# Kernel optimization log

Hardware: AMD Instinct MI355X
Metric: run time of the kernel (lower is better)

Reference implementation:

```python
import jax, jax.numpy as jnp
import numpy as np

NEG_SLOPE = 0.2  # PyG GATConv default negative_slope


def _add_self_loops(edge_index, num_nodes):
    # PyG GATConv add_self_loops=True default
    loop = jnp.arange(num_nodes, dtype=edge_index.dtype)
    src = jnp.concatenate([edge_index[0], loop])
    dst = jnp.concatenate([edge_index[1], loop])
    return src, dst


def _gat_layer(x, src, dst, W, att_src, att_dst, bias, heads, out_ch):
    """One PyG-style GATConv layer (concat=True).
    x: [N, F_in]; W: [F_in, heads*out_ch]; att_*: [heads, out_ch]; bias: [heads*out_ch].
    """
    N = x.shape[0]
    h = (x @ W).reshape(N, heads, out_ch)               # [N, H, C]
    a_src = jnp.einsum('nhc,hc->nh', h, att_src)        # [N, H]
    a_dst = jnp.einsum('nhc,hc->nh', h, att_dst)        # [N, H]
    logits = jax.nn.leaky_relu(a_src[src] + a_dst[dst], NEG_SLOPE)  # [E, H]
    # segment softmax over destination neighborhoods
    m = jax.ops.segment_max(logits, dst, num_segments=N)            # [N, H]
    e = jnp.exp(logits - m[dst])                                     # [E, H]
    s = jax.ops.segment_sum(e, dst, num_segments=N)                  # [N, H]
    alpha = e / s[dst]                                               # [E, H]
    # scatter-aggregate weighted source features
    out = jax.ops.segment_sum(alpha[:, :, None] * h[src], dst, num_segments=N)  # [N, H, C]
    return out.reshape(N, heads * out_ch) + bias


def setup_inputs() -> dict:
    key = jax.random.key(0)
    ks = jax.random.split(key, 10)
    N, E = 50000, 800000
    F_in, HID, H, NC = 128, 64, 4, 10
    x = jax.random.normal(ks[0], (N, F_in), dtype=jnp.float32)
    edge_index = jax.random.randint(ks[1], (2, E), 0, N, dtype=jnp.int64)
    sc1 = 1.0 / np.sqrt(F_in)
    sc2 = 1.0 / np.sqrt(HID * H)
    return {
        'x': x,
        'edge_index': edge_index,
        'W1': jax.random.normal(ks[2], (F_in, H * HID), dtype=jnp.float32) * sc1,
        'att_src1': jax.random.normal(ks[3], (H, HID), dtype=jnp.float32) * sc1,
        'att_dst1': jax.random.normal(ks[4], (H, HID), dtype=jnp.float32) * sc1,
        'b1': jnp.zeros((H * HID,), dtype=jnp.float32),
        'W2': jax.random.normal(ks[5], (H * HID, NC), dtype=jnp.float32) * sc2,
        'att_src2': jax.random.normal(ks[6], (1, NC), dtype=jnp.float32) * sc2,
        'att_dst2': jax.random.normal(ks[7], (1, NC), dtype=jnp.float32) * sc2,
        'b2': jnp.zeros((NC,), dtype=jnp.float32),
    }


def reference(x, edge_index, W1, att_src1, att_dst1, b1, W2, att_src2, att_dst2, b2):
    N = x.shape[0]
    src, dst = _add_self_loops(edge_index, N)
    h = _gat_layer(x, src, dst, W1, att_src1, att_dst1, b1, heads=4, out_ch=64)
    h = jax.nn.elu(h)
    out = _gat_layer(h, src, dst, W2, att_src2, att_dst2, b2, heads=1, out_ch=10)
    return out
```

## Files before the change

### kernel.cpp

```cpp
#include <hip/hip_runtime.h>
#include <hip/hip_fp16.h>
#include <math.h>

#define NEG_SLOPE 0.2f
#define LOG2E 1.44269504088896f

#if __has_builtin(__builtin_amdgcn_exp2f)
#define EXP2(x) __builtin_amdgcn_exp2f(x)
#else
#define EXP2(x) exp2f(x)
#endif

typedef _Float16 half8 __attribute__((ext_vector_type(8)));
typedef float floatx4 __attribute__((ext_vector_type(4)));

__global__ __launch_bounds__(256) void prep1(const float* __restrict__ W1,
                                             half8* __restrict__ Bpack,
                                             int* __restrict__ deg, int N) {
  if (blockIdx.x < 16) {
    int tid = blockIdx.x * 256 + threadIdx.x;
    int l = tid & 63;
    int ksnt = tid >> 6;
    int ks = ksnt & 3;
    int nt = ksnt >> 2;
    int col = nt * 16 + (l & 15);
    int krow = ks * 32 + (l >> 4) * 8;
    half8 v;
#pragma unroll
    for (int j = 0; j < 8; j++) v[j] = (_Float16)W1[(krow + j) * 256 + col];
    Bpack[tid] = v;
  } else {
    int i = (blockIdx.x - 16) * 256 + threadIdx.x;
    if (i < N) deg[i] = 0;
  }
}

__global__ __launch_bounds__(256) void phase2(
    const float* __restrict__ x, const half8* __restrict__ Bpack,
    const float* __restrict__ att_s, const float* __restrict__ att_d,
    unsigned char* __restrict__ h1q, float* __restrict__ a1sx,
    float* __restrict__ a1d,
    const int* __restrict__ dst, int* __restrict__ deg, int* __restrict__ rank,
    int N, int E, int gemmBlocks, int histBlocks) {
  if ((int)blockIdx.x >= gemmBlocks) {
    int b = blockIdx.x - gemmBlocks;
    for (int e = b * 256 + threadIdx.x; e < E; e += histBlocks * 256)
      rank[e] = atomicAdd(deg + dst[e], 1);
    return;
  }
  const int wave = threadIdx.x >> 6, lane = threadIdx.x & 63;
  const int quad = lane >> 4, li = lane & 15;
  const int n0 = (blockIdx.x * 4 + wave) * 16;
  if (n0 >= N) return;
  floatx4 acc[16];
#pragma unroll
  for (int t = 0; t < 16; t++) acc[t] = (floatx4){0.f, 0.f, 0.f, 0.f};
  const float* xrow = x + (size_t)(n0 + li) * 128;
#pragma unroll
  for (int ks = 0; ks < 4; ks++) {
    float4 xa = *(const float4*)(xrow + ks * 32 + quad * 8);
    float4 xb = *(const float4*)(xrow + ks * 32 + quad * 8 + 4);
    half8 a;
    a[0] = (_Float16)xa.x; a[1] = (_Float16)xa.y;
    a[2] = (_Float16)xa.z; a[3] = (_Float16)xa.w;
    a[4] = (_Float16)xb.x; a[5] = (_Float16)xb.y;
    a[6] = (_Float16)xb.z; a[7] = (_Float16)xb.w;
#pragma unroll
    for (int nt = 0; nt < 16; nt++) {
      half8 b = Bpack[(nt * 4 + ks) * 64 + lane];
      acc[nt] = __builtin_amdgcn_mfma_f32_16x16x32_f16(a, b, acc[nt], 0, 0, 0);
    }
  }
#pragma unroll
  for (int r = 0; r < 4; r++) {
    float m = 0.f;
#pragma unroll
    for (int nt = 0; nt < 16; nt++) m = fmaxf(m, fabsf(acc[nt][r]));
#pragma unroll
    for (int off = 8; off > 0; off >>= 1) m = fmaxf(m, __shfl_xor(m, off, 16));
    m = fmaxf(m, 1e-8f);
    float inv = 127.0f / m;
    int node = n0 + quad * 4 + r;
    if (li == 0) a1sx[(size_t)node * 8 + 4] = m * (1.0f / 127.0f);
#pragma unroll
    for (int nt = 0; nt < 16; nt++) {
      h1q[(size_t)node * 256 + nt * 16 + li] =
          (unsigned char)(int)(fmaf(acc[nt][r], inv, 128.5f));
    }
  }
  float as_f[16], ad_f[16];
#pragma unroll
  for (int nt = 0; nt < 16; nt++) {
    as_f[nt] = att_s[nt * 16 + li];
    ad_f[nt] = att_d[nt * 16 + li];
  }
#pragma unroll
  for (int r = 0; r < 4; r++) {
    int node = n0 + quad * 4 + r;
#pragma unroll
    for (int h = 0; h < 4; h++) {
      float vs = 0.f, vd = 0.f;
#pragma unroll
      for (int ntl = 0; ntl < 4; ntl++) {
        int nt = h * 4 + ntl;
        vs = fmaf(acc[nt][r], as_f[nt], vs);
        vd = fmaf(acc[nt][r], ad_f[nt], vd);
      }
#pragma unroll
      for (int off = 8; off > 0; off >>= 1) {
        vs += __shfl_down(vs, off, 16);
        vd += __shfl_down(vd, off, 16);
      }
      if (li == 0) {
        a1sx[(size_t)node * 8 + h] = vs * LOG2E;
        a1d[node * 4 + h] = vd * LOG2E;
      }
    }
  }
}

__global__ void scan_local(const int* __restrict__ deg, int* __restrict__ excl,
                           int* __restrict__ bsum, int N) {
  __shared__ int s[256];
  int i = blockIdx.x * 256 + threadIdx.x;
  int v = (i < N) ? deg[i] + 1 : 0;
  s[threadIdx.x] = v;
  __syncthreads();
  for (int off = 1; off < 256; off <<= 1) {
    int t = (threadIdx.x >= off) ? s[threadIdx.x - off] : 0;
    __syncthreads();
    s[threadIdx.x] += t;
    __syncthreads();
  }
  if (i < N) excl[i] = s[threadIdx.x] - v;
  if (threadIdx.x == 255) bsum[blockIdx.x] = s[255];
}

__global__ void scan_add2(const int* __restrict__ excl, const int* __restrict__ bsum,
                          int* __restrict__ rowptr, int* __restrict__ elist,
                          int N, int nb) {
  __shared__ int s[256];
  int v = (threadIdx.x < nb) ? bsum[threadIdx.x] : 0;
  s[threadIdx.x] = v;
  __syncthreads();
  for (int off = 1; off < 256; off <<= 1) {
    int t = (threadIdx.x >= off) ? s[threadIdx.x - off] : 0;
    __syncthreads();
    s[threadIdx.x] += t;
    __syncthreads();
  }
  __syncthreads();
  int base = (blockIdx.x > 0) ? s[blockIdx.x - 1] : 0;
  int i = blockIdx.x * 256 + threadIdx.x;
  if (i < N) {
    int r = excl[i] + base;
    rowptr[i] = r;
    elist[r] = i;
  }
  if (blockIdx.x == 0 && threadIdx.x == 0) rowptr[N] = s[nb - 1];
}

__global__ void scatter2(const int* __restrict__ src, const int* __restrict__ dst,
                         const int* __restrict__ rank, const int* __restrict__ rowptr,
                         int* __restrict__ elist, int E) {
  int e = blockIdx.x * 256 + threadIdx.x;
  if (e >= E) return;
  elist[rowptr[dst[e]] + 1 + rank[e]] = src[e];
}

__global__ __launch_bounds__(256) void agg1_fused(
    const int* __restrict__ rowptr, const int* __restrict__ elist,
    const unsigned char* __restrict__ h1q, const float* __restrict__ a1sx,
    const float* __restrict__ a1d,
    const float* __restrict__ b1, const float* __restrict__ W2,
    const float* __restrict__ as2, const float* __restrict__ ad2,
    __half* __restrict__ h2, int N) {
  __shared__ float w2s[64 * 41];
  __shared__ float cbuf[8][256];
  const int t = threadIdx.x;
  for (int i = t; i < 2560; i += 256) {
    int ch = i / 10, jj = i - ch * 10;
    w2s[(ch >> 2) * 41 + (ch & 3) * 10 + jj] = W2[i];
  }

  const int wave = t >> 6, lane = t & 63;
  const int half = lane >> 5, l32 = lane & 31;
  const int slot = wave * 2 + half;
  const int n = blockIdx.x * 8 + slot;
  const bool act = n < N;
  const int row = act ? rowptr[n] : 0;
  const int deg = act ? rowptr[n + 1] - row : 0;
  const int* el = elist + row;
  const int hidx = l32 >> 3;
  const float adh = act ? a1d[n * 4 + hidx] : 0.f;

  float den = 0.f, T = 0.f;
  float acc[8];
#pragma unroll
  for (int k = 0; k < 8; k++) acc[k] = 0.f;

  int j = 0;
  for (; j + 4 <= deg; j += 4) {
    int ss[4];
    float lv[4], sc[4];
    uint2 qv[4];
#pragma unroll
    for (int u = 0; u < 4; u++) ss[u] = el[j + u];
#pragma unroll
    for (int u = 0; u < 4; u++) {
      const float* mp = a1sx + (size_t)ss[u] * 8;
      lv[u] = mp[hidx];
      sc[u] = mp[4];
      qv[u] = *(const uint2*)(h1q + (size_t)ss[u] * 256 + l32 * 8);
    }
#pragma unroll
    for (int u = 0; u < 4; u++) {
      float l = lv[u] + adh;
      float e = EXP2(fmaxf(l, NEG_SLOPE * l));
      den += e;
      float se = e * sc[u];
      T += se;
      unsigned int a = qv[u].x, b = qv[u].y;
      acc[0] = fmaf((float)(a & 0xffu), se, acc[0]);
      acc[1] = fmaf((float)((a >> 8) & 0xffu), se, acc[1]);
      acc[2] = fmaf((float)((a >> 16) & 0xffu), se, acc[2]);
      acc[3] = fmaf((float)(a >> 24), se, acc[3]);
      acc[4] = fmaf((float)(b & 0xffu), se, acc[4]);
      acc[5] = fmaf((float)((b >> 8) & 0xffu), se, acc[5]);
      acc[6] = fmaf((float)((b >> 16) & 0xffu), se, acc[6]);
      acc[7] = fmaf((float)(b >> 24), se, acc[7]);
    }
  }
  for (; j < deg; j++) {
    int s0 = el[j];
    const float* mp = a1sx + (size_t)s0 * 8;
    float l0 = mp[hidx] + adh;
    float sc0 = mp[4];
    uint2 q0 = *(const uint2*)(h1q + (size_t)s0 * 256 + l32 * 8);
    float e0 = EXP2(fmaxf(l0, NEG_SLOPE * l0));
    den += e0;
    float se = e0 * sc0;
    T += se;
    unsigned int a = q0.x, b = q0.y;
    acc[0] = fmaf((float)(a & 0xffu), se, acc[0]);
    acc[1] = fmaf((float)((a >> 8) & 0xffu), se, acc[1]);
    acc[2] = fmaf((float)((a >> 16) & 0xffu), se, acc[2]);
    acc[3] = fmaf((float)(a >> 24), se, acc[3]);
    acc[4] = fmaf((float)(b & 0xffu), se, acc[4]);
    acc[5] = fmaf((float)((b >> 8) & 0xffu), se, acc[5]);
    acc[6] = fmaf((float)((b >> 16) & 0xffu), se, acc[6]);
    acc[7] = fmaf((float)(b >> 24), se, acc[7]);
  }

  if (act) {
    float inv = 1.0f / den;
    float corr = 128.0f * T;
    float4 v0 = make_float4((acc[0] - corr) * inv, (acc[1] - corr) * inv,
                            (acc[2] - corr) * inv, (acc[3] - corr) * inv);
    float4 v1 = make_float4((acc[4] - corr) * inv, (acc[5] - corr) * inv,
                            (acc[6] - corr) * inv, (acc[7] - corr) * inv);
    *(float4*)&cbuf[slot][l32 * 8] = v0;
    *(float4*)&cbuf[slot][l32 * 8 + 4] = v1;
  }
  __syncthreads();

  float4 bb = *(const float4*)(b1 + lane * 4);
  const float* w0 = w2s + lane * 41;
#pragma unroll
  for (int pp = 0; pp < 2; pp++) {
    int slot2 = wave * 2 + pp;
    int n2 = blockIdx.x * 8 + slot2;
    if (n2 >= N) continue;
    float4 cv = *(const float4*)&cbuf[slot2][lane * 4];
    float c0 = cv.x + bb.x;
    float c1 = cv.y + bb.y;
    float c2 = cv.z + bb.z;
    float c3 = cv.w + bb.w;
    c0 = c0 > 0.f ? c0 : expm1f(c0);
    c1 = c1 > 0.f ? c1 : expm1f(c1);
    c2 = c2 > 0.f ? c2 : expm1f(c2);
    c3 = c3 > 0.f ? c3 : expm1f(c3);
    float p[10];
#pragma unroll
    for (int jj = 0; jj < 10; jj++)
      p[jj] = fmaf(c0, w0[jj],
              fmaf(c1, w0[10 + jj], fmaf(c2, w0[20 + jj], c3 * w0[30 + jj])));
#pragma unroll
    for (int jj = 0; jj < 10; jj++) {
#pragma unroll
      for (int off = 32; off > 0; off >>= 1) p[jj] += __shfl_down(p[jj], off, 64);
    }
    if (lane == 0) {
      float ds = 0.f, dd = 0.f;
#pragma unroll
      for (int jj = 0; jj < 10; jj++) {
        h2[(size_t)n2 * 16 + jj] = __float2half(p[jj]);
        ds = fmaf(p[jj], as2[jj], ds);
        dd = fmaf(p[jj], ad2[jj], dd);
      }
      float* ft = (float*)(h2 + (size_t)n2 * 16);
      ft[5] = ds * LOG2E;
      ft[6] = dd * LOG2E;
    }
  }
}

__global__ __launch_bounds__(256) void agg2_csr(
    const int* __restrict__ rowptr, const int* __restrict__ elist,
    const __half* __restrict__ h2, const float* __restrict__ b2,
    float* __restrict__ out, int N) {
  int wave = threadIdx.x >> 6, lane = threadIdx.x & 63;
  int n = blockIdx.x * 4 + wave;
  if (n >= N) return;
  int row = rowptr[n];
  int deg = rowptr[n + 1] - row;
  const int* el = elist + row;
  const float* hf = (const float*)h2;
  float ad = hf[(size_t)n * 8 + 6];
  int g = lane / 5;
  int c2 = lane - g * 5;
  float den = 0.f, ax = 0.f, ay = 0.f;
  if (g < 12) {
    int jj = g;
    for (; jj + 12 < deg; jj += 24) {
      int sA = el[jj], sB = el[jj + 12];
      float lA = hf[(size_t)sA * 8 + 5] + ad;
      float lB = hf[(size_t)sB * 8 + 5] + ad;
      __half2 hA = *(const __half2*)(h2 + (size_t)sA * 16 + c2 * 2);
      __half2 hB = *(const __half2*)(h2 + (size_t)sB * 16 + c2 * 2);
      float eA = EXP2(fmaxf(lA, NEG_SLOPE * lA));
      float eB = EXP2(fmaxf(lB, NEG_SLOPE * lB));
      den += eA + eB;
      float2 fA = __half22float2(hA);
      float2 fB = __half22float2(hB);
      ax = fmaf(eA, fA.x, fmaf(eB, fB.x, ax));
      ay = fmaf(eA, fA.y, fmaf(eB, fB.y, ay));
    }
    for (; jj < deg; jj += 12) {
      int s = el[jj];
      float l = hf[(size_t)s * 8 + 5] + ad;
      __half2 hv = *(const __half2*)(h2 + (size_t)s * 16 + c2 * 2);
      float ev = EXP2(fmaxf(l, NEG_SLOPE * l));
      den += ev;
      float2 f = __half22float2(hv);
      ax = fmaf(ev, f.x, ax);
      ay = fmaf(ev, f.y, ay);
    }
  }
  ax += __shfl_down(ax, 30, 64);
  ay += __shfl_down(ay, 30, 64);
  den += __shfl_down(den, 30, 64);
  ax += __shfl_down(ax, 10, 64) + __shfl_down(ax, 20, 64);
  ay += __shfl_down(ay, 10, 64) + __shfl_down(ay, 20, 64);
  den += __shfl_down(den, 10, 64) + __shfl_down(den, 20, 64);
  ax += __shfl_down(ax, 5, 64);
  ay += __shfl_down(ay, 5, 64);
  den += __shfl_down(den, 5, 64);
  if (lane < 5) {
    float inv = 1.0f / den;
    float2 bb = *(const float2*)(b2 + lane * 2);
    float2 o = make_float2(fmaf(ax, inv, bb.x), fmaf(ay, inv, bb.y));
    *(float2*)(out + (size_t)n * 10 + lane * 2) = o;
  }
}

extern "C" void kernel_launch(void* const* d_in, const int* in_sizes, int n_in,
                              void* d_out, int out_size, void* d_ws, size_t ws_size,
                              hipStream_t stream) {
  const float* x = (const float*)d_in[0];
  const int* ei = (const int*)d_in[1];
  const float* W1 = (const float*)d_in[2];
  const float* as1 = (const float*)d_in[3];
  const float* ad1 = (const float*)d_in[4];
  const float* b1 = (const float*)d_in[5];
  const float* W2 = (const float*)d_in[6];
  const float* as2 = (const float*)d_in[7];
  const float* ad2 = (const float*)d_in[8];
  const float* b2 = (const float*)d_in[9];
  float* out = (float*)d_out;

  const int N = in_sizes[0] / 128;
  const int E = in_sizes[1] / 2;
  const int* srcp = ei;
  const int* dstp = ei + E;

  char* ws = (char*)d_ws;
  size_t off = 0;
  auto alloc = [&](size_t nbytes) {
    char* p = ws + off;
    off += (nbytes + 255) & ~(size_t)255;
    return p;
  };
  unsigned char* h1q = (unsigned char*)alloc((size_t)N * 256);
  float* a1sx = (float*)alloc((size_t)N * 8 * 4);
  half8* Bpack = (half8*)alloc((size_t)4096 * 16);
  float* a1d = (float*)alloc((size_t)N * 4 * 4);
  __half* h2 = (__half*)alloc((size_t)N * 16 * 2);
  int* deg = (int*)alloc((size_t)N * 4);
  int* excl = (int*)alloc((size_t)N * 4);
  int* bsum = (int*)alloc(256 * 4);
  int* rowptr = (int*)alloc((size_t)(N + 1) * 4);
  int* rank = (int*)alloc((size_t)E * 4);
  int* elist = (int*)alloc((size_t)(E + (size_t)N) * 4);

  const int nb = (N + 255) / 256;
  const int gemmBlocks = (N / 16 + 3) / 4;
  const int histBlocks = 512;

  prep1<<<16 + nb, 256, 0, stream>>>(W1, Bpack, deg, N);
  phase2<<<gemmBlocks + histBlocks, 256, 0, stream>>>(
      x, Bpack, as1, ad1, h1q, a1sx, a1d, dstp, deg, rank, N, E,
      gemmBlocks, histBlocks);
  scan_local<<<nb, 256, 0, stream>>>(deg, excl, bsum, N);
  scan_add2<<<nb, 256, 0, stream>>>(excl, bsum, rowptr, elist, N, nb);
  scatter2<<<(E + 255) / 256, 256, 0, stream>>>(srcp, dstp, rank, rowptr, elist, E);
  agg1_fused<<<(N + 7) / 8, 256, 0, stream>>>(rowptr, elist, h1q, a1sx, a1d,
                                              b1, W2, as2, ad2, h2, N);
  agg2_csr<<<(N + 3) / 4, 256, 0, stream>>>(rowptr, elist, h2, b2, out, N);
}
```

Measured before the change: 249.8 us.

## Embed per-source attention scalars into a 32-byte edge list record

Each CSR edge entry grows from a bare source index to a 32-byte record. The record holds the source's four head attention logits, its quantization scale and a precomputed byte offset into h1q. These are written during the scatter. The aggregation kernels then read the record sequentially instead of doing a dependent random gather into a1sx, and agg2 reuses the offset (shifted) to address h2. The trade is 8x more edge-list memory traffic and a larger scatter write, in exchange for one fewer dependent random load per edge; a launch_bounds occupancy hint is also added.

Result: slower. 264.0 us (+5.7%).

```diff
diff --git a/kernel.cpp b/kernel.cpp
--- a/kernel.cpp
+++ b/kernel.cpp
@@ -137,7 +137,8 @@
 }
 
 __global__ void scan_add2(const int* __restrict__ excl, const int* __restrict__ bsum,
-                          int* __restrict__ rowptr, int* __restrict__ elist,
+                          const float* __restrict__ a1sx,
+                          int* __restrict__ rowptr, char* __restrict__ elist2,
                           int N, int nb) {
   __shared__ int s[256];
   int v = (threadIdx.x < nb) ? bsum[threadIdx.x] : 0;
@@ -155,23 +156,33 @@
   if (i < N) {
     int r = excl[i] + base;
     rowptr[i] = r;
-    elist[r] = i;
+    float4 m0 = *(const float4*)(a1sx + (size_t)i * 8);
+    float sc = a1sx[(size_t)i * 8 + 4];
+    float4* ep = (float4*)(elist2 + (size_t)r * 32);
+    ep[0] = m0;
+    ep[1] = make_float4(sc, __int_as_float(i * 256), 0.f, 0.f);
   }
   if (blockIdx.x == 0 && threadIdx.x == 0) rowptr[N] = s[nb - 1];
 }
 
 __global__ void scatter2(const int* __restrict__ src, const int* __restrict__ dst,
                          const int* __restrict__ rank, const int* __restrict__ rowptr,
-                         int* __restrict__ elist, int E) {
+                         const float* __restrict__ a1sx, char* __restrict__ elist2,
+                         int E) {
   int e = blockIdx.x * 256 + threadIdx.x;
   if (e >= E) return;
-  elist[rowptr[dst[e]] + 1 + rank[e]] = src[e];
-}
-
-__global__ __launch_bounds__(256) void agg1_fused(
-    const int* __restrict__ rowptr, const int* __restrict__ elist,
-    const unsigned char* __restrict__ h1q, const float* __restrict__ a1sx,
-    const float* __restrict__ a1d,
+  int s = src[e];
+  int r = rowptr[dst[e]] + 1 + rank[e];
+  float4 m0 = *(const float4*)(a1sx + (size_t)s * 8);
+  float sc = a1sx[(size_t)s * 8 + 4];
+  float4* ep = (float4*)(elist2 + (size_t)r * 32);
+  ep[0] = m0;
+  ep[1] = make_float4(sc, __int_as_float(s * 256), 0.f, 0.f);
+}
+
+__global__ __launch_bounds__(256, 4) void agg1_fused(
+    const int* __restrict__ rowptr, const char* __restrict__ elist2,
+    const unsigned char* __restrict__ h1q, const float* __restrict__ a1d,
     const float* __restrict__ b1, const float* __restrict__ W2,
     const float* __restrict__ as2, const float* __restrict__ ad2,
     __half* __restrict__ h2, int N) {
@@ -190,10 +201,12 @@
   const bool act = n < N;
   const int row = act ? rowptr[n] : 0;
   const int deg = act ? rowptr[n + 1] - row : 0;
-  const int* el = elist + row;
   const int hidx = l32 >> 3;
   const float adh = act ? a1d[n * 4 + hidx] : 0.f;
 
+  const float4* eb = (const float4*)(elist2) + (size_t)row * 2;
+  const unsigned char* h1ql = h1q + l32 * 8;
+
   float den = 0.f, T = 0.f;
   float acc[8];
 #pragma unroll
@@ -201,24 +214,24 @@
 
   int j = 0;
   for (; j + 4 <= deg; j += 4) {
-    int ss[4];
-    float lv[4], sc[4];
+    float4 ea[4], es[4];
     uint2 qv[4];
 #pragma unroll
-    for (int u = 0; u < 4; u++) ss[u] = el[j + u];
-#pragma unroll
     for (int u = 0; u < 4; u++) {
-      const float* mp = a1sx + (size_t)ss[u] * 8;
-      lv[u] = mp[hidx];
-      sc[u] = mp[4];
-      qv[u] = *(const uint2*)(h1q + (size_t)ss[u] * 256 + l32 * 8);
-    }
+      ea[u] = eb[(size_t)(j + u) * 2];
+      es[u] = eb[(size_t)(j + u) * 2 + 1];
+    }
+#pragma unroll
+    for (int u = 0; u < 4; u++)
+      qv[u] = *(const uint2*)(h1ql + (size_t)__float_as_uint(es[u].y));
 #pragma unroll
     for (int u = 0; u < 4; u++) {
-      float l = lv[u] + adh;
+      float lh = (hidx & 2) ? ((hidx & 1) ? ea[u].w : ea[u].z)
+                            : ((hidx & 1) ? ea[u].y : ea[u].x);
+      float l = lh + adh;
       float e = EXP2(fmaxf(l, NEG_SLOPE * l));
       den += e;
-      float se = e * sc[u];
+      float se = e * es[u].x;
       T += se;
       unsigned int a = qv[u].x, b = qv[u].y;
       acc[0] = fmaf((float)(a & 0xffu), se, acc[0]);
@@ -232,14 +245,15 @@
     }
   }
   for (; j < deg; j++) {
-    int s0 = el[j];
-    const float* mp = a1sx + (size_t)s0 * 8;
-    float l0 = mp[hidx] + adh;
-    float sc0 = mp[4];
-    uint2 q0 = *(const uint2*)(h1q + (size_t)s0 * 256 + l32 * 8);
+    float4 ea = eb[(size_t)j * 2];
+    float4 es = eb[(size_t)j * 2 + 1];
+    uint2 q0 = *(const uint2*)(h1ql + (size_t)__float_as_uint(es.y));
+    float lh = (hidx & 2) ? ((hidx & 1) ? ea.w : ea.z)
+                          : ((hidx & 1) ? ea.y : ea.x);
+    float l0 = lh + adh;
     float e0 = EXP2(fmaxf(l0, NEG_SLOPE * l0));
     den += e0;
-    float se = e0 * sc0;
+    float se = e0 * es.x;
     T += se;
     unsigned int a = q0.x, b = q0.y;
     acc[0] = fmaf((float)(a & 0xffu), se, acc[0]);
@@ -306,7 +320,7 @@
 }
 
 __global__ __launch_bounds__(256) void agg2_csr(
-    const int* __restrict__ rowptr, const int* __restrict__ elist,
+    const int* __restrict__ rowptr, const char* __restrict__ elist2,
     const __half* __restrict__ h2, const float* __restrict__ b2,
     float* __restrict__ out, int N) {
   int wave = threadIdx.x >> 6, lane = threadIdx.x & 63;
@@ -314,7 +328,8 @@
   if (n >= N) return;
   int row = rowptr[n];
   int deg = rowptr[n + 1] - row;
-  const int* el = elist + row;
+  const char* el2 = elist2 + (size_t)row * 32 + 20;
+  const char* h2b = (const char*)h2;
   const float* hf = (const float*)h2;
   float ad = hf[(size_t)n * 8 + 6];
   int g = lane / 5;
@@ -323,11 +338,14 @@
   if (g < 12) {
     int jj = g;
     for (; jj + 12 < deg; jj += 24) {
-      int sA = el[jj], sB = el[jj + 12];
-      float lA = hf[(size_t)sA * 8 + 5] + ad;
-      float lB = hf[(size_t)sB * 8 + 5] + ad;
-      __half2 hA = *(const __half2*)(h2 + (size_t)sA * 16 + c2 * 2);
-      __half2 hB = *(const __half2*)(h2 + (size_t)sB * 16 + c2 * 2);
+      unsigned oA = __float_as_uint(*(const float*)(el2 + (size_t)jj * 32));
+      unsigned oB = __float_as_uint(*(const float*)(el2 + (size_t)(jj + 12) * 32));
+      const float* rA = (const float*)(h2b + (oA >> 3));
+      const float* rB = (const float*)(h2b + (oB >> 3));
+      float lA = rA[5] + ad;
+      float lB = rB[5] + ad;
+      __half2 hA = *(const __half2*)((const char*)rA + c2 * 4);
+      __half2 hB = *(const __half2*)((const char*)rB + c2 * 4);
       float eA = EXP2(fmaxf(lA, NEG_SLOPE * lA));
       float eB = EXP2(fmaxf(lB, NEG_SLOPE * lB));
       den += eA + eB;
@@ -337,9 +355,10 @@
       ay = fmaf(eA, fA.y, fmaf(eB, fB.y, ay));
     }
     for (; jj < deg; jj += 12) {
-      int s = el[jj];
-      float l = hf[(size_t)s * 8 + 5] + ad;
-      __half2 hv = *(const __half2*)(h2 + (size_t)s * 16 + c2 * 2);
+      unsigned o = __float_as_uint(*(const float*)(el2 + (size_t)jj * 32));
+      const float* r = (const float*)(h2b + (o >> 3));
+      float l = r[5] + ad;
+      __half2 hv = *(const __half2*)((const char*)r + c2 * 4);
       float ev = EXP2(fmaxf(l, NEG_SLOPE * l));
       den += ev;
       float2 f = __half22float2(hv);
@@ -401,7 +420,7 @@
   int* bsum = (int*)alloc(256 * 4);
   int* rowptr = (int*)alloc((size_t)(N + 1) * 4);
   int* rank = (int*)alloc((size_t)E * 4);
-  int* elist = (int*)alloc((size_t)(E + (size_t)N) * 4);
+  char* elist2 = (char*)alloc((size_t)(E + (size_t)N) * 32);
 
   const int nb = (N + 255) / 256;
   const int gemmBlocks = (N / 16 + 3) / 4;
@@ -412,9 +431,10 @@
       x, Bpack, as1, ad1, h1q, a1sx, a1d, dstp, deg, rank, N, E,
       gemmBlocks, histBlocks);
   scan_local<<<nb, 256, 0, stream>>>(deg, excl, bsum, N);
-  scan_add2<<<nb, 256, 0, stream>>>(excl, bsum, rowptr, elist, N, nb);
-  scatter2<<<(E + 255) / 256, 256, 0, stream>>>(srcp, dstp, rank, rowptr, elist, E);
-  agg1_fused<<<(N + 7) / 8, 256, 0, stream>>>(rowptr, elist, h1q, a1sx, a1d,
+  scan_add2<<<nb, 256, 0, stream>>>(excl, bsum, a1sx, rowptr, elist2, N, nb);
+  scatter2<<<(E + 255) / 256, 256, 0, stream>>>(srcp, dstp, rank, rowptr, a1sx,
+                                                elist2, E);
+  agg1_fused<<<(N + 7) / 8, 256, 0, stream>>>(rowptr, elist2, h1q, a1d,
                                               b1, W2, as2, ad2, h2, N);
-  agg2_csr<<<(N + 3) / 4, 256, 0, stream>>>(rowptr, elist, h2, b2, out, N);
-}
+  agg2_csr<<<(N + 3) / 4, 256, 0, stream>>>(rowptr, elist2, h2, b2, out, N);
+}
```

## Partially sort CSR neighbor lists by source tile for gather locality

Applied to the files above, without the earlier changes.

Splits each destination's degree counter into eight buckets keyed by the high bits of the source index. The scatter then places edges grouped by source tile within each row, so neighbor lists are roughly ordered by source. This is meant to improve cache locality of the h1q and h2 feature gathers in the aggregation kernels. In exchange it uses a degree array eight times larger, with more zeroing, a wider read in the scan, and extra prefix work per edge in the scatter. Correctness depends on N fitting within eight tiles of 8192 sources.

Result: no change. 250.3 us (+0.2%).

```diff
diff --git a/kernel.cpp b/kernel.cpp
--- a/kernel.cpp
+++ b/kernel.cpp
@@ -13,6 +13,9 @@
 
 typedef _Float16 half8 __attribute__((ext_vector_type(8)));
 typedef float floatx4 __attribute__((ext_vector_type(4)));
+
+#define SRC_TILE_SHIFT 13
+#define NTILES 8
 
 __global__ __launch_bounds__(256) void prep1(const float* __restrict__ W1,
                                              half8* __restrict__ Bpack,
@@ -31,7 +34,7 @@
     Bpack[tid] = v;
   } else {
     int i = (blockIdx.x - 16) * 256 + threadIdx.x;
-    if (i < N) deg[i] = 0;
+    if (i < N * NTILES) deg[i] = 0;
   }
 }
 
@@ -40,12 +43,15 @@
     const float* __restrict__ att_s, const float* __restrict__ att_d,
     unsigned char* __restrict__ h1q, float* __restrict__ a1sx,
     float* __restrict__ a1d,
-    const int* __restrict__ dst, int* __restrict__ deg, int* __restrict__ rank,
+    const int* __restrict__ src, const int* __restrict__ dst,
+    int* __restrict__ deg, int* __restrict__ rank,
     int N, int E, int gemmBlocks, int histBlocks) {
   if ((int)blockIdx.x >= gemmBlocks) {
     int b = blockIdx.x - gemmBlocks;
-    for (int e = b * 256 + threadIdx.x; e < E; e += histBlocks * 256)
-      rank[e] = atomicAdd(deg + dst[e], 1);
+    for (int e = b * 256 + threadIdx.x; e < E; e += histBlocks * 256) {
+      int tile = src[e] >> SRC_TILE_SHIFT;
+      rank[e] = atomicAdd(deg + dst[e] * NTILES + tile, 1);
+    }
     return;
   }
   const int wave = threadIdx.x >> 6, lane = threadIdx.x & 63;
@@ -123,7 +129,12 @@
                            int* __restrict__ bsum, int N) {
   __shared__ int s[256];
   int i = blockIdx.x * 256 + threadIdx.x;
-  int v = (i < N) ? deg[i] + 1 : 0;
+  int v = 0;
+  if (i < N) {
+    const int4* dp = (const int4*)(deg + (size_t)i * NTILES);
+    int4 c0 = dp[0], c1 = dp[1];
+    v = c0.x + c0.y + c0.z + c0.w + c1.x + c1.y + c1.z + c1.w + 1;
+  }
   s[threadIdx.x] = v;
   __syncthreads();
   for (int off = 1; off < 256; off <<= 1) {
@@ -162,10 +173,19 @@
 
 __global__ void scatter2(const int* __restrict__ src, const int* __restrict__ dst,
                          const int* __restrict__ rank, const int* __restrict__ rowptr,
-                         int* __restrict__ elist, int E) {
+                         const int* __restrict__ deg, int* __restrict__ elist, int E) {
   int e = blockIdx.x * 256 + threadIdx.x;
   if (e >= E) return;
-  elist[rowptr[dst[e]] + 1 + rank[e]] = src[e];
+  int s = src[e];
+  int d = dst[e];
+  int tile = s >> SRC_TILE_SHIFT;
+  const int4* dp = (const int4*)(deg + (size_t)d * NTILES);
+  int4 c0 = dp[0], c1 = dp[1];
+  int cnt[8] = {c0.x, c0.y, c0.z, c0.w, c1.x, c1.y, c1.z, c1.w};
+  int pre = 0;
+#pragma unroll
+  for (int t = 0; t < 7; t++) pre += (t < tile) ? cnt[t] : 0;
+  elist[rowptr[d] + 1 + pre + rank[e]] = s;
 }
 
 __global__ __launch_bounds__(256) void agg1_fused(
@@ -396,7 +416,7 @@
   half8* Bpack = (half8*)alloc((size_t)4096 * 16);
   float* a1d = (float*)alloc((size_t)N * 4 * 4);
   __half* h2 = (__half*)alloc((size_t)N * 16 * 2);
-  int* deg = (int*)alloc((size_t)N * 4);
+  int* deg = (int*)alloc((size_t)N * NTILES * 4);
   int* excl = (int*)alloc((size_t)N * 4);
   int* bsum = (int*)alloc(256 * 4);
   int* rowptr = (int*)alloc((size_t)(N + 1) * 4);
@@ -404,16 +424,18 @@
   int* elist = (int*)alloc((size_t)(E + (size_t)N) * 4);
 
   const int nb = (N + 255) / 256;
+  const int nbz = (N * NTILES + 255) / 256;
   const int gemmBlocks = (N / 16 + 3) / 4;
   const int histBlocks = 512;
 
-  prep1<<<16 + nb, 256, 0, stream>>>(W1, Bpack, deg, N);
+  prep1<<<16 + nbz, 256, 0, stream>>>(W1, Bpack, deg, N);
   phase2<<<gemmBlocks + histBlocks, 256, 0, stream>>>(
-      x, Bpack, as1, ad1, h1q, a1sx, a1d, dstp, deg, rank, N, E,
+      x, Bpack, as1, ad1, h1q, a1sx, a1d, srcp, dstp, deg, rank, N, E,
       gemmBlocks, histBlocks);
   scan_local<<<nb, 256, 0, stream>>>(deg, excl, bsum, N);
   scan_add2<<<nb, 256, 0, stream>>>(excl, bsum, rowptr, elist, N, nb);
-  scatter2<<<(E + 255) / 256, 256, 0, stream>>>(srcp, dstp, rank, rowptr, elist, E);
+  scatter2<<<(E + 255) / 256, 256, 0, stream>>>(srcp, dstp, rank, rowptr, deg,
+                                                elist, E);
   agg1_fused<<<(N + 7) / 8, 256, 0, stream>>>(rowptr, elist, h1q, a1sx, a1d,
                                               b1, W2, as2, ad2, h2, N);
   agg2_csr<<<(N + 3) / 4, 256, 0, stream>>>(rowptr, elist, h2, b2, out, N);
```

## Split layer-1 aggregation per head with XCD-aware mapping and degree-sorted nodes

Applied to the files above, without the earlier changes.

Stores quantized h1 and per-head logit/scale in head-major planes so each head's gather touches a smaller contiguous array. Blocks are mapped so each XCD pair handles one head, which keeps that head's plane resident in the local L2. Nodes are counting-sorted by degree so wavefronts see balanced work. The layer-2 projection now goes through per-head partial sums and a new combine kernel, which adds launches, an N×40 float intermediate and atomics for binning.

After: 486.3 us. 1.95x slower.

```diff
diff --git a/kernel.cpp b/kernel.cpp
--- a/kernel.cpp
+++ b/kernel.cpp
@@ -16,7 +16,7 @@
 
 __global__ __launch_bounds__(256) void prep1(const float* __restrict__ W1,
                                              half8* __restrict__ Bpack,
-                                             int* __restrict__ deg, int N) {
+                                             int* __restrict__ zbuf, int N) {
   if (blockIdx.x < 16) {
     int tid = blockIdx.x * 256 + threadIdx.x;
     int l = tid & 63;
@@ -31,14 +31,14 @@
     Bpack[tid] = v;
   } else {
     int i = (blockIdx.x - 16) * 256 + threadIdx.x;
-    if (i < N) deg[i] = 0;
+    if (i < N + 256) zbuf[i] = 0;
   }
 }
 
 __global__ __launch_bounds__(256) void phase2(
     const float* __restrict__ x, const half8* __restrict__ Bpack,
     const float* __restrict__ att_s, const float* __restrict__ att_d,
-    unsigned char* __restrict__ h1q, float* __restrict__ a1sx,
+    unsigned char* __restrict__ h1qh, float2* __restrict__ a1h,
     float* __restrict__ a1d,
     const int* __restrict__ dst, int* __restrict__ deg, int* __restrict__ rank,
     int N, int E, int gemmBlocks, int histBlocks) {
@@ -52,6 +52,7 @@
   const int quad = lane >> 4, li = lane & 15;
   const int n0 = (blockIdx.x * 4 + wave) * 16;
   if (n0 >= N) return;
+  const size_t N64 = (size_t)N * 64;
   floatx4 acc[16];
 #pragma unroll
   for (int t = 0; t < 16; t++) acc[t] = (floatx4){0.f, 0.f, 0.f, 0.f};
@@ -71,6 +72,7 @@
       acc[nt] = __builtin_amdgcn_mfma_f32_16x16x32_f16(a, b, acc[nt], 0, 0, 0);
     }
   }
+  float scv[4];
 #pragma unroll
   for (int r = 0; r < 4; r++) {
     float m = 0.f;
@@ -80,11 +82,11 @@
     for (int off = 8; off > 0; off >>= 1) m = fmaxf(m, __shfl_xor(m, off, 16));
     m = fmaxf(m, 1e-8f);
     float inv = 127.0f / m;
+    scv[r] = m * (1.0f / 127.0f);
     int node = n0 + quad * 4 + r;
-    if (li == 0) a1sx[(size_t)node * 8 + 4] = m * (1.0f / 127.0f);
 #pragma unroll
     for (int nt = 0; nt < 16; nt++) {
-      h1q[(size_t)node * 256 + nt * 16 + li] =
+      h1qh[(size_t)(nt >> 2) * N64 + (size_t)node * 64 + (nt & 3) * 16 + li] =
           (unsigned char)(int)(fmaf(acc[nt][r], inv, 128.5f));
     }
   }
@@ -112,18 +114,19 @@
         vd += __shfl_down(vd, off, 16);
       }
       if (li == 0) {
-        a1sx[(size_t)node * 8 + h] = vs * LOG2E;
+        a1h[(size_t)h * N + node] = make_float2(vs * LOG2E, scv[r]);
         a1d[node * 4 + h] = vd * LOG2E;
       }
     }
   }
 }
 
-__global__ void scan_local(const int* __restrict__ deg, int* __restrict__ excl,
-                           int* __restrict__ bsum, int N) {
+__global__ void scan_local(const int* __restrict__ deg, int* __restrict__ binCnt,
+                           int* __restrict__ excl, int* __restrict__ bsum, int N) {
   __shared__ int s[256];
   int i = blockIdx.x * 256 + threadIdx.x;
   int v = (i < N) ? deg[i] + 1 : 0;
+  if (i < N) atomicAdd(binCnt + min(deg[i], 255), 1);
   s[threadIdx.x] = v;
   __syncthreads();
   for (int off = 1; off < 256; off <<= 1) {
@@ -134,6 +137,20 @@
   }
   if (i < N) excl[i] = s[threadIdx.x] - v;
   if (threadIdx.x == 255) bsum[blockIdx.x] = s[255];
+}
+
+__global__ void binscan(const int* __restrict__ binCnt, int* __restrict__ cursor) {
+  __shared__ int s[256];
+  int v = binCnt[threadIdx.x];
+  s[threadIdx.x] = v;
+  __syncthreads();
+  for (int off = 1; off < 256; off <<= 1) {
+    int t = (threadIdx.x >= off) ? s[threadIdx.x - off] : 0;
+    __syncthreads();
+    s[threadIdx.x] += t;
+    __syncthreads();
+  }
+  cursor[threadIdx.x] = s[threadIdx.x] - v;
 }
 
 __global__ void scan_add2(const int* __restrict__ excl, const int* __restrict__ bsum,
@@ -168,59 +185,66 @@
   elist[rowptr[dst[e]] + 1 + rank[e]] = src[e];
 }
 
-__global__ __launch_bounds__(256) void agg1_fused(
+__global__ void place(const int* __restrict__ deg, int* __restrict__ cursor,
+                      int* __restrict__ perm, int N) {
+  int i = blockIdx.x * 256 + threadIdx.x;
+  if (i >= N) return;
+  perm[atomicAdd(cursor + min(deg[i], 255), 1)] = i;
+}
+
+__global__ __launch_bounds__(256) void agg1_heads(
     const int* __restrict__ rowptr, const int* __restrict__ elist,
-    const unsigned char* __restrict__ h1q, const float* __restrict__ a1sx,
-    const float* __restrict__ a1d,
-    const float* __restrict__ b1, const float* __restrict__ W2,
-    const float* __restrict__ as2, const float* __restrict__ ad2,
-    __half* __restrict__ h2, int N) {
-  __shared__ float w2s[64 * 41];
-  __shared__ float cbuf[8][256];
+    const int* __restrict__ perm,
+    const unsigned char* __restrict__ h1qh, const float2* __restrict__ a1h,
+    const float* __restrict__ a1d, const float* __restrict__ b1,
+    const float* __restrict__ W2, float* __restrict__ phuf, int N) {
+  __shared__ float w2s[256 * 11];
   const int t = threadIdx.x;
   for (int i = t; i < 2560; i += 256) {
     int ch = i / 10, jj = i - ch * 10;
-    w2s[(ch >> 2) * 41 + (ch & 3) * 10 + jj] = W2[i];
+    w2s[ch * 11 + jj] = W2[i];
   }
 
   const int wave = t >> 6, lane = t & 63;
-  const int half = lane >> 5, l32 = lane & 31;
-  const int slot = wave * 2 + half;
-  const int n = blockIdx.x * 8 + slot;
-  const bool act = n < N;
+  const int s = lane >> 3;
+  const int k = lane & 7;
+  const int xcd = blockIdx.x & 7;
+  const int head = xcd >> 1, sub = xcd & 1;
+  const int chunk = (blockIdx.x >> 3) * 2 + sub;
+  const int gidx = chunk * 32 + wave * 8 + s;
+  const bool act = gidx < N;
+  const int n = act ? perm[gidx] : 0;
   const int row = act ? rowptr[n] : 0;
-  const int deg = act ? rowptr[n + 1] - row : 0;
-  const int* el = elist + row;
-  const int hidx = l32 >> 3;
-  const float adh = act ? a1d[n * 4 + hidx] : 0.f;
+  const int en = act ? rowptr[n + 1] : 0;
+  const float adh = act ? a1d[n * 4 + head] : 0.f;
+  const float2* mh = a1h + (size_t)head * N;
+  const unsigned char* hb = h1qh + (size_t)head * N * 64 + k * 8;
 
   float den = 0.f, T = 0.f;
   float acc[8];
 #pragma unroll
-  for (int k = 0; k < 8; k++) acc[k] = 0.f;
-
-  int j = 0;
-  for (; j + 4 <= deg; j += 4) {
+  for (int u = 0; u < 8; u++) acc[u] = 0.f;
+
+  int j = row;
+  for (; j + 4 <= en; j += 4) {
     int ss[4];
-    float lv[4], sc[4];
+    float2 mv[4];
     uint2 qv[4];
 #pragma unroll
-    for (int u = 0; u < 4; u++) ss[u] = el[j + u];
+    for (int u = 0; u < 4; u++) ss[u] = elist[j + u];
 #pragma unroll
     for (int u = 0; u < 4; u++) {
-      const float* mp = a1sx + (size_t)ss[u] * 8;
-      lv[u] = mp[hidx];
-      sc[u] = mp[4];
-      qv[u] = *(const uint2*)(h1q + (size_t)ss[u] * 256 + l32 * 8);
+      mv[u] = mh[ss[u]];
+      qv[u] = *(const uint2*)(hb + ((size_t)ss[u] << 6));
     }
 #pragma unroll
     for (int u = 0; u < 4; u++) {
-      float l = lv[u] + adh;
+      float l = mv[u].x + adh;
       float e = EXP2(fmaxf(l, NEG_SLOPE * l));
       den += e;
-      float se = e * sc[u];
+      float se = e * mv[u].y;
       T += se;
-      unsigned int a = qv[u].x, b = qv[u].y;
+      unsigned a = qv[u].x, b = qv[u].y;
       acc[0] = fmaf((float)(a & 0xffu), se, acc[0]);
       acc[1] = fmaf((float)((a >> 8) & 0xffu), se, acc[1]);
       acc[2] = fmaf((float)((a >> 16) & 0xffu), se, acc[2]);
@@ -231,17 +255,16 @@
       acc[7] = fmaf((float)(b >> 24), se, acc[7]);
     }
   }
-  for (; j < deg; j++) {
-    int s0 = el[j];
-    const float* mp = a1sx + (size_t)s0 * 8;
-    float l0 = mp[hidx] + adh;
-    float sc0 = mp[4];
-    uint2 q0 = *(const uint2*)(h1q + (size_t)s0 * 256 + l32 * 8);
+  for (; j < en; j++) {
+    int s0 = elist[j];
+    float2 mv = mh[s0];
+    uint2 q0 = *(const uint2*)(hb + ((size_t)s0 << 6));
+    float l0 = mv.x + adh;
     float e0 = EXP2(fmaxf(l0, NEG_SLOPE * l0));
     den += e0;
-    float se = e0 * sc0;
+    float se = e0 * mv.y;
     T += se;
-    unsigned int a = q0.x, b = q0.y;
+    unsigned a = q0.x, b = q0.y;
     acc[0] = fmaf((float)(a & 0xffu), se, acc[0]);
     acc[1] = fmaf((float)((a >> 8) & 0xffu), se, acc[1]);
     acc[2] = fmaf((float)((a >> 16) & 0xffu), se, acc[2]);
@@ -252,57 +275,57 @@
     acc[7] = fmaf((float)(b >> 24), se, acc[7]);
   }
 
-  if (act) {
-    float inv = 1.0f / den;
-    float corr = 128.0f * T;
-    float4 v0 = make_float4((acc[0] - corr) * inv, (acc[1] - corr) * inv,
-                            (acc[2] - corr) * inv, (acc[3] - corr) * inv);
-    float4 v1 = make_float4((acc[4] - corr) * inv, (acc[5] - corr) * inv,
-                            (acc[6] - corr) * inv, (acc[7] - corr) * inv);
-    *(float4*)&cbuf[slot][l32 * 8] = v0;
-    *(float4*)&cbuf[slot][l32 * 8 + 4] = v1;
-  }
   __syncthreads();
 
-  float4 bb = *(const float4*)(b1 + lane * 4);
-  const float* w0 = w2s + lane * 41;
-#pragma unroll
-  for (int pp = 0; pp < 2; pp++) {
-    int slot2 = wave * 2 + pp;
-    int n2 = blockIdx.x * 8 + slot2;
-    if (n2 >= N) continue;
-    float4 cv = *(const float4*)&cbuf[slot2][lane * 4];
-    float c0 = cv.x + bb.x;
-    float c1 = cv.y + bb.y;
-    float c2 = cv.z + bb.z;
-    float c3 = cv.w + bb.w;
-    c0 = c0 > 0.f ? c0 : expm1f(c0);
-    c1 = c1 > 0.f ? c1 : expm1f(c1);
-    c2 = c2 > 0.f ? c2 : expm1f(c2);
-    c3 = c3 > 0.f ? c3 : expm1f(c3);
-    float p[10];
-#pragma unroll
-    for (int jj = 0; jj < 10; jj++)
-      p[jj] = fmaf(c0, w0[jj],
-              fmaf(c1, w0[10 + jj], fmaf(c2, w0[20 + jj], c3 * w0[30 + jj])));
-#pragma unroll
-    for (int jj = 0; jj < 10; jj++) {
-#pragma unroll
-      for (int off = 32; off > 0; off >>= 1) p[jj] += __shfl_down(p[jj], off, 64);
-    }
-    if (lane == 0) {
-      float ds = 0.f, dd = 0.f;
-#pragma unroll
-      for (int jj = 0; jj < 10; jj++) {
-        h2[(size_t)n2 * 16 + jj] = __float2half(p[jj]);
-        ds = fmaf(p[jj], as2[jj], ds);
-        dd = fmaf(p[jj], ad2[jj], dd);
-      }
-      float* ft = (float*)(h2 + (size_t)n2 * 16);
-      ft[5] = ds * LOG2E;
-      ft[6] = dd * LOG2E;
-    }
-  }
+  float bbv[8];
+  {
+    float4 b0 = *(const float4*)(b1 + head * 64 + k * 8);
+    float4 b1v = *(const float4*)(b1 + head * 64 + k * 8 + 4);
+    bbv[0] = b0.x; bbv[1] = b0.y; bbv[2] = b0.z; bbv[3] = b0.w;
+    bbv[4] = b1v.x; bbv[5] = b1v.y; bbv[6] = b1v.z; bbv[7] = b1v.w;
+  }
+  float inv = act ? 1.0f / den : 0.f;
+  float corr = 128.0f * T;
+  float pv[10];
+#pragma unroll
+  for (int jj = 0; jj < 10; jj++) pv[jj] = 0.f;
+#pragma unroll
+  for (int u = 0; u < 8; u++) {
+    float c = (acc[u] - corr) * inv + bbv[u];
+    c = c > 0.f ? c : expm1f(c);
+    const float* wrow = w2s + (head * 64 + k * 8 + u) * 11;
+#pragma unroll
+    for (int jj = 0; jj < 10; jj++) pv[jj] = fmaf(c, wrow[jj], pv[jj]);
+  }
+#pragma unroll
+  for (int off = 4; off > 0; off >>= 1) {
+#pragma unroll
+    for (int jj = 0; jj < 10; jj++) pv[jj] += __shfl_down(pv[jj], off, 8);
+  }
+  if (act && k == 0) {
+    float* pp = phuf + ((size_t)n * 4 + head) * 10;
+#pragma unroll
+    for (int jj = 0; jj < 10; jj++) pp[jj] = pv[jj];
+  }
+}
+
+__global__ __launch_bounds__(256) void combine(
+    const float* __restrict__ phuf, const float* __restrict__ as2,
+    const float* __restrict__ ad2, __half* __restrict__ h2, int N) {
+  int n = blockIdx.x * 256 + threadIdx.x;
+  if (n >= N) return;
+  const float* pp = phuf + (size_t)n * 40;
+  float ds = 0.f, dd = 0.f;
+#pragma unroll
+  for (int jj = 0; jj < 10; jj++) {
+    float p = pp[jj] + pp[10 + jj] + pp[20 + jj] + pp[30 + jj];
+    h2[(size_t)n * 16 + jj] = __float2half(p);
+    ds = fmaf(p, as2[jj], ds);
+    dd = fmaf(p, ad2[jj], dd);
+  }
+  float* ft = (float*)(h2 + (size_t)n * 16);
+  ft[5] = ds * LOG2E;
+  ft[6] = dd * LOG2E;
 }
 
 __global__ __launch_bounds__(256) void agg2_csr(
@@ -391,30 +414,41 @@
     off += (nbytes + 255) & ~(size_t)255;
     return p;
   };
-  unsigned char* h1q = (unsigned char*)alloc((size_t)N * 256);
-  float* a1sx = (float*)alloc((size_t)N * 8 * 4);
+  unsigned char* h1qh = (unsigned char*)alloc((size_t)N * 256);
+  float2* a1h = (float2*)alloc((size_t)N * 4 * 8);
   half8* Bpack = (half8*)alloc((size_t)4096 * 16);
   float* a1d = (float*)alloc((size_t)N * 4 * 4);
+  float* phuf = (float*)alloc((size_t)N * 40 * 4);
   __half* h2 = (__half*)alloc((size_t)N * 16 * 2);
-  int* deg = (int*)alloc((size_t)N * 4);
+  int* zbuf = (int*)alloc((size_t)(N + 256) * 4);
+  int* deg = zbuf;
+  int* binCnt = zbuf + N;
+  int* cursor = (int*)alloc(256 * 4);
   int* excl = (int*)alloc((size_t)N * 4);
   int* bsum = (int*)alloc(256 * 4);
   int* rowptr = (int*)alloc((size_t)(N + 1) * 4);
+  int* perm = (int*)alloc((size_t)N * 4);
   int* rank = (int*)alloc((size_t)E * 4);
   int* elist = (int*)alloc((size_t)(E + (size_t)N) * 4);
 
   const int nb = (N + 255) / 256;
+  const int nbz = (N + 256 + 255) / 256;
   const int gemmBlocks = (N / 16 + 3) / 4;
   const int histBlocks = 512;
-
-  prep1<<<16 + nb, 256, 0, stream>>>(W1, Bpack, deg, N);
+  const int chunks = (N + 31) / 32;
+  const int hgrid = ((chunks + 1) / 2) * 8;
+
+  prep1<<<16 + nbz, 256, 0, stream>>>(W1, Bpack, zbuf, N);
   phase2<<<gemmBlocks + histBlocks, 256, 0, stream>>>(
-      x, Bpack, as1, ad1, h1q, a1sx, a1d, dstp, deg, rank, N, E,
+      x, Bpack, as1, ad1, h1qh, a1h, a1d, dstp, deg, rank, N, E,
       gemmBlocks, histBlocks);
-  scan_local<<<nb, 256, 0, stream>>>(deg, excl, bsum, N);
+  scan_local<<<nb, 256, 0, stream>>>(deg, binCnt, excl, bsum, N);
+  binscan<<<1, 256, 0, stream>>>(binCnt, cursor);
   scan_add2<<<nb, 256, 0, stream>>>(excl, bsum, rowptr, elist, N, nb);
   scatter2<<<(E + 255) / 256, 256, 0, stream>>>(srcp, dstp, rank, rowptr, elist, E);
-  agg1_fused<<<(N + 7) / 8, 256, 0, stream>>>(rowptr, elist, h1q, a1sx, a1d,
-                                              b1, W2, as2, ad2, h2, N);
+  place<<<nb, 256, 0, stream>>>(deg, cursor, perm, N);
+  agg1_heads<<<hgrid, 256, 0, stream>>>(rowptr, elist, perm, h1qh, a1h, a1d,
+                                        b1, W2, phuf, N);
+  combine<<<(N + 255) / 256, 256, 0, stream>>>(phuf, as2, ad2, h2, N);
   agg2_csr<<<(N + 3) / 4, 256, 0, stream>>>(rowptr, elist, h2, b2, out, N);
 }
```
